# Kernel tuning notes

Measured on AMD Instinct MI355X. Metric: run time of the kernel, lower is better.

Reference implementation:

```python
import jax, jax.numpy as jnp
import numpy as np

N = 2_097_152
EPS = 1e-6


def _tri(x):
    # triangleWave (period 2), maps R -> [0, 1]; applied to 'normalize=True' tables
    return 2.0 * jnp.abs(x / 2.0 - jnp.floor(x / 2.0 + 0.5))


def _grid2d(uv, table, bilinear, normalize):
    # uv: (N,2) in [0,1); table: (U,V,L)
    t = _tri(table) if normalize else table
    U, V, _ = t.shape
    u = jnp.clip(uv[:, 0], 0.0, 1.0 - EPS) * (U - 1)
    v = jnp.clip(uv[:, 1], 0.0, 1.0 - EPS) * (V - 1)
    if bilinear:
        u0 = jnp.floor(u)
        v0 = jnp.floor(v)
        fu = (u - u0)[:, None]
        fv = (v - v0)[:, None]
        u0i = u0.astype(jnp.int32)
        v0i = v0.astype(jnp.int32)
        u1i = jnp.minimum(u0i + 1, U - 1)
        v1i = jnp.minimum(v0i + 1, V - 1)
        return (t[u0i, v0i] * (1 - fu) * (1 - fv)
                + t[u1i, v0i] * fu * (1 - fv)
                + t[u0i, v1i] * (1 - fu) * fv
                + t[u1i, v1i] * fu * fv)
    return t[jnp.round(u).astype(jnp.int32), jnp.round(v).astype(jnp.int32)]


def _grid1d(u, table, bilinear, normalize):
    # u: (N,) in [0,1); table: (U,L)
    t = _tri(table) if normalize else table
    U, _ = t.shape
    uu = jnp.clip(u, 0.0, 1.0 - EPS) * (U - 1)
    if bilinear:
        u0 = jnp.floor(uu)
        fu = (uu - u0)[:, None]
        u0i = u0.astype(jnp.int32)
        u1i = jnp.minimum(u0i + 1, U - 1)
        return t[u0i] * (1 - fu) + t[u1i] * fu
    return t[jnp.round(uu).astype(jnp.int32)]


def setup_inputs() -> dict:
    key = jax.random.key(0)
    ks = jax.random.split(key, 17)
    mk = lambda i, shape: jax.random.uniform(ks[i], shape, dtype=jnp.float32)
    names = ["roughNoh", "anisoToh", "nDotLV", "tDotLV", "metalLoh",
             "subCg", "spst", "shst", "lumCs"]
    d = {n: mk(i, (N, 2)) for i, n in enumerate(names)}
    d["tabRAEnc"] = mk(9, (2048, 2048, 2))
    d["tabCgEnc"] = mk(10, (2048, 1))
    d["tabRSEnc"] = mk(11, (64, 64, 3))
    d["tabRADec"] = mk(12, (48, 48, 3))
    d["tabCgDec"] = mk(13, (96, 2))
    d["tabLVR"] = mk(14, (32, 32, 1))
    d["tabLV"] = mk(15, (32, 32, 4))
    d["tabNHL"] = mk(16, (32, 32, 4))
    return d


def reference(roughNoh, anisoToh, nDotLV, tDotLV, metalLoh, subCg, spst, shst,
              lumCs, tabRAEnc, tabCgEnc, tabRSEnc, tabRADec, tabCgDec,
              tabLVR, tabLV, tabNHL):
    raIn = jnp.stack((roughNoh[:, 0], anisoToh[:, 0]), axis=1)  # (N,2)
    metallicity = metalLoh[:, 0]
    # ---- encoder: LUT lookups + elementwise mixing coefficients ----
    ra = _grid2d(raIn, tabRAEnc, bilinear=False, normalize=True)           # (N,2)
    cg = _grid1d(subCg[:, 1], tabCgEnc, bilinear=False, normalize=True)    # (N,1)
    rsEnc = _grid2d(jnp.concatenate((raIn[:, 0:1], subCg[:, 0:1]), axis=1),
                    tabRSEnc, bilinear=True, normalize=True)               # (N,3)
    cd = (1 - metallicity) * lumCs[:, 0]
    cm0 = (spst[:, 0] * 0.1 * (1 - metallicity) * spst[:, 1]
           + metallicity * lumCs[:, 0])[:, None]
    cm1 = (spst[:, 0] * 0.1 * (1 - metallicity) * (1 - spst[:, 1]))[:, None]
    cs0 = (shst[:, 0] * (1 - metallicity) * shst[:, 1])[:, None]
    cs1 = (shst[:, 0] * (1 - metallicity) * (1 - shst[:, 1]))[:, None]
    cc = (0.25 * 0.25 * lumCs[:, 1])[:, None]
    rsCd = rsEnc * cd[:, None]                                             # (N,3)
    # ---- decoder LUTs ----
    raCoefs = _grid2d(ra, tabRADec, bilinear=True, normalize=False)        # (N,3)
    cgCoefs = _grid1d(cg[:, 0], tabCgDec, bilinear=True, normalize=False)  # (N,2)
    vTerm = _grid2d(jnp.concatenate((nDotLV[:, 0:1] * nDotLV[:, 1:2],
                                     ra[:, 0:1]), axis=1),
                    tabLVR, bilinear=True, normalize=True)                 # (N,1)
    nlvCoefs = _grid2d(nDotLV, tabLV, bilinear=True, normalize=True)       # (N,4)
    nhlCoefs = _grid2d(jnp.stack((metalLoh[:, 1], nDotLV[:, 0]), axis=1),
                       tabNHL, bilinear=True, normalize=True)              # (N,4)
    # ---- elementwise shading combination ----
    noh2 = roughNoh[:, 1] ** 2
    den = raCoefs[:, 0] * anisoToh[:, 1] ** 2 + raCoefs[:, 1] * noh2 + raCoefs[:, 2]
    dTerm = (0.25 / (nDotLV[:, 1] * den ** 2))[:, None]
    x = (rsCd[:, 0:1] * metalLoh[:, 1:2] * nlvCoefs[:, 1:2]
         + rsCd[:, 1:2] * nlvCoefs[:, 2:3]
         + rsCd[:, 2:3] * nlvCoefs[:, 3:4]
         + cm0 * vTerm * nhlCoefs[:, 2:3] * dTerm
         + cs0 * nhlCoefs[:, 0:1])
    y = (((1 - cm1) * nhlCoefs[:, 3:4] + cm1) * vTerm * dTerm
         + cs1 * nhlCoefs[:, 0:1]
         + cc * nhlCoefs[:, 1:2] * nlvCoefs[:, 0:1]
           / (nDotLV[:, 1] * (cgCoefs[:, 0] * noh2 + cgCoefs[:, 1]))[:, None])
    return jnp.concatenate((x, y), axis=1)  # (N,2)
```

## Files before the change

### kernel.cpp

```cpp
#include <hip/hip_runtime.h>
#include <hip/hip_fp16.h>

#define CLIP_HI (1.0f - 1e-6f)

typedef float f4v __attribute__((ext_vector_type(4)));

__device__ __forceinline__ float tri_(float x) {
    return 2.0f * fabsf(x * 0.5f - floorf(x * 0.5f + 0.5f));
}

__device__ __forceinline__ float clamp01(float x) {
    return fminf(fmaxf(x, 0.0f), CLIP_HI);
}

__device__ __forceinline__ float4 nt_load4(const float* p) {
    f4v v = __builtin_nontemporal_load((const f4v*)p);
    return make_float4(v.x, v.y, v.z, v.w);
}
__device__ __forceinline__ void nt_store4(float* p, float4 v) {
    f4v t = {v.x, v.y, v.z, v.w};
    __builtin_nontemporal_store(t, (f4v*)p);
}

struct H4 { __half2 xy, zw; };

struct BW {
    int i00, i10, i01, i11;
    float w00, w10, w01, w11;
};

template <int U, int V>
__device__ __forceinline__ BW bw2d(float uc, float vc) {
    float u = clamp01(uc) * (float)(U - 1);
    float v = clamp01(vc) * (float)(V - 1);
    float u0f = floorf(u), v0f = floorf(v);
    float fu = u - u0f, fv = v - v0f;
    int u0 = (int)u0f, v0 = (int)v0f;
    int u1 = min(u0 + 1, U - 1);
    int v1 = min(v0 + 1, V - 1);
    BW r;
    r.i00 = u0 * V + v0;
    r.i10 = u1 * V + v0;
    r.i01 = u0 * V + v1;
    r.i11 = u1 * V + v1;
    float gu = 1.0f - fu, gv = 1.0f - fv;
    r.w00 = gu * gv; r.w10 = fu * gv; r.w01 = gu * fv; r.w11 = fu * fv;
    return r;
}

__device__ __forceinline__ float4 h4_blend(H4 A, H4 B, H4 C, H4 D, const BW& b) {
    float2 Axy = __half22float2(A.xy), Azw = __half22float2(A.zw);
    float2 Bxy = __half22float2(B.xy), Bzw = __half22float2(B.zw);
    float2 Cxy = __half22float2(C.xy), Czw = __half22float2(C.zw);
    float2 Dxy = __half22float2(D.xy), Dzw = __half22float2(D.zw);
    return make_float4(
        Axy.x * b.w00 + Bxy.x * b.w10 + Cxy.x * b.w01 + Dxy.x * b.w11,
        Axy.y * b.w00 + Bxy.y * b.w10 + Cxy.y * b.w01 + Dxy.y * b.w11,
        Azw.x * b.w00 + Bzw.x * b.w10 + Czw.x * b.w01 + Dzw.x * b.w11,
        Azw.y * b.w00 + Bzw.y * b.w10 + Czw.y * b.w01 + Dzw.y * b.w11);
}

__global__ __launch_bounds__(256) void prep_rs_kernel(const float* __restrict__ t,
                                                      H4* __restrict__ o) {
    int j = blockIdx.x * 256 + threadIdx.x;
    if (j < 64 * 64) {
        float a = tri_(t[j * 3 + 0]);
        float b = tri_(t[j * 3 + 1]);
        float c = tri_(t[j * 3 + 2]);
        H4 h;
        h.xy = __floats2half2_rn(a, b);
        h.zw = __floats2half2_rn(c, 0.0f);
        o[j] = h;
    }
}

template <bool USE_WS>
__device__ __forceinline__ float2 shade(
    float rNx, float rNy, float aTx, float aTy, float nLVx, float nLVy,
    float mLx, float mLy, float sCx, float sCy, float spx, float spy,
    float shx, float shy, float lCx, float lCy,
    const float* __restrict__ tabRAEnc, const float* __restrict__ tabRSEnc,
    const H4* __restrict__ rsPacked,
    const float* sRADec, const float2* sCgDec, const float* sCgEnc,
    const float* sLVR, const H4* sLV, const H4* sNHL)
{
    int ui = (int)rintf(clamp01(rNx) * 2047.0f);
    int vi = (int)rintf(clamp01(aTx) * 2047.0f);
    float2 raT = ((const float2*)tabRAEnc)[ui * 2048 + vi];

    float rs0, rs1, rs2;
    {
        BW b = bw2d<64, 64>(rNx, sCx);
        if constexpr (USE_WS) {
            float4 r = h4_blend(rsPacked[b.i00], rsPacked[b.i10],
                                rsPacked[b.i01], rsPacked[b.i11], b);
            rs0 = r.x; rs1 = r.y; rs2 = r.z;
        } else {
            const float* p00 = tabRSEnc + b.i00 * 3;
            const float* p10 = tabRSEnc + b.i10 * 3;
            const float* p01 = tabRSEnc + b.i01 * 3;
            const float* p11 = tabRSEnc + b.i11 * 3;
            rs0 = tri_(p00[0]) * b.w00 + tri_(p10[0]) * b.w10 + tri_(p01[0]) * b.w01 + tri_(p11[0]) * b.w11;
            rs1 = tri_(p00[1]) * b.w00 + tri_(p10[1]) * b.w10 + tri_(p01[1]) * b.w01 + tri_(p11[1]) * b.w11;
            rs2 = tri_(p00[2]) * b.w00 + tri_(p10[2]) * b.w10 + tri_(p01[2]) * b.w01 + tri_(p11[2]) * b.w11;
        }
    }

    float cgC0, cgC1;
    {
        float cg = sCgEnc[(int)rintf(clamp01(sCy) * 2047.0f)];
        float u = clamp01(cg) * 95.0f;
        float u0f = floorf(u);
        float fu = u - u0f;
        int u0 = (int)u0f;
        int u1 = min(u0 + 1, 95);
        float2 a = sCgDec[u0];
        float2 b = sCgDec[u1];
        cgC0 = a.x * (1.0f - fu) + b.x * fu;
        cgC1 = a.y * (1.0f - fu) + b.y * fu;
    }

    float4 nlv, nhl;
    {
        BW b = bw2d<32, 32>(nLVx, nLVy);
        nlv = h4_blend(sLV[b.i00], sLV[b.i10], sLV[b.i01], sLV[b.i11], b);
    }
    {
        BW b = bw2d<32, 32>(mLy, nLVx);
        nhl = h4_blend(sNHL[b.i00], sNHL[b.i10], sNHL[b.i01], sNHL[b.i11], b);
    }

    float ra0 = tri_(raT.x);
    float ra1 = tri_(raT.y);

    float raC0, raC1, raC2;
    {
        BW b = bw2d<48, 48>(ra0, ra1);
        const float* p00 = &sRADec[b.i00 * 3];
        const float* p10 = &sRADec[b.i10 * 3];
        const float* p01 = &sRADec[b.i01 * 3];
        const float* p11 = &sRADec[b.i11 * 3];
        raC0 = p00[0] * b.w00 + p10[0] * b.w10 + p01[0] * b.w01 + p11[0] * b.w11;
        raC1 = p00[1] * b.w00 + p10[1] * b.w10 + p01[1] * b.w01 + p11[1] * b.w11;
        raC2 = p00[2] * b.w00 + p10[2] * b.w10 + p01[2] * b.w01 + p11[2] * b.w11;
    }

    float vTerm;
    {
        BW b = bw2d<32, 32>(nLVx * nLVy, ra0);
        vTerm = sLVR[b.i00] * b.w00 + sLVR[b.i10] * b.w10 +
                sLVR[b.i01] * b.w01 + sLVR[b.i11] * b.w11;
    }

    float met = mLx;
    float om  = 1.0f - met;
    float cd  = om * lCx;
    float cm0 = spx * 0.1f * om * spy + met * lCx;
    float cm1 = spx * 0.1f * om * (1.0f - spy);
    float cs0 = shx * om * shy;
    float cs1 = shx * om * (1.0f - shy);
    float cc  = 0.0625f * lCy;

    float noh2 = rNy * rNy;
    float den  = raC0 * aTy * aTy + raC1 * noh2 + raC2;
    float dTerm = 0.25f / (nLVy * den * den);

    float x = rs0 * cd * mLy * nlv.y + rs1 * cd * nlv.z + rs2 * cd * nlv.w
            + cm0 * vTerm * nhl.z * dTerm + cs0 * nhl.x;

    float y = ((1.0f - cm1) * nhl.w + cm1) * vTerm * dTerm
            + cs1 * nhl.x
            + cc * nhl.y * nlv.x / (nLVy * (cgC0 * noh2 + cgC1));

    return make_float2(x, y);
}

template <bool USE_WS>
__global__ __launch_bounds__(1024, 8) void disney_main(
    const float* __restrict__ roughNoh,
    const float* __restrict__ anisoToh,
    const float* __restrict__ nDotLV,
    const float* __restrict__ metalLoh,
    const float* __restrict__ subCg,
    const float* __restrict__ spst,
    const float* __restrict__ shst,
    const float* __restrict__ lumCs,
    const float* __restrict__ tabRAEnc,
    const float* __restrict__ tabCgEnc,
    const float* __restrict__ tabRSEnc,
    const H4*    __restrict__ rsPacked,
    const float* __restrict__ tabRADec,
    const float* __restrict__ tabCgDec,
    const float* __restrict__ tabLVR,
    const float* __restrict__ tabLV,
    const float* __restrict__ tabNHL,
    float* __restrict__ out,
    int n)
{
    __shared__ float  sRADec[48 * 48 * 3];
    __shared__ float2 sCgDec[96];
    __shared__ float  sCgEnc[2048];
    __shared__ float  sLVR[1024];
    __shared__ H4     sLV[1024];
    __shared__ H4     sNHL[1024];

    int tid = threadIdx.x;

    for (int j = tid; j < 48 * 48 * 3; j += 1024) sRADec[j] = tabRADec[j];
    if (tid < 96) sCgDec[tid] = ((const float2*)tabCgDec)[tid];
    sCgEnc[tid]        = tri_(tabCgEnc[tid]);
    sCgEnc[tid + 1024] = tri_(tabCgEnc[tid + 1024]);
    sLVR[tid] = tri_(tabLVR[tid]);
    {
        float4 v = ((const float4*)tabLV)[tid];
        H4 h; h.xy = __floats2half2_rn(tri_(v.x), tri_(v.y));
              h.zw = __floats2half2_rn(tri_(v.z), tri_(v.w));
        sLV[tid] = h;
    }
    {
        float4 v = ((const float4*)tabNHL)[tid];
        H4 h; h.xy = __floats2half2_rn(tri_(v.x), tri_(v.y));
              h.zw = __floats2half2_rn(tri_(v.z), tri_(v.w));
        sNHL[tid] = h;
    }
    __syncthreads();

    int p = blockIdx.x * 1024 + tid;
    int e0 = 2 * p;
    if (e0 >= n) return;
    bool has2 = (e0 + 1) < n;

    float4 rN  = nt_load4(roughNoh + 4 * p);
    float4 aT  = nt_load4(anisoToh + 4 * p);
    float4 nLV = nt_load4(nDotLV   + 4 * p);
    float4 mL  = nt_load4(metalLoh + 4 * p);
    float4 sC  = nt_load4(subCg    + 4 * p);
    float4 sp  = nt_load4(spst     + 4 * p);
    float4 sh  = nt_load4(shst     + 4 * p);
    float4 lC  = nt_load4(lumCs    + 4 * p);

    float2 r0 = shade<USE_WS>(rN.x, rN.y, aT.x, aT.y, nLV.x, nLV.y,
                              mL.x, mL.y, sC.x, sC.y, sp.x, sp.y,
                              sh.x, sh.y, lC.x, lC.y,
                              tabRAEnc, tabRSEnc, rsPacked,
                              sRADec, sCgDec, sCgEnc, sLVR, sLV, sNHL);
    if (has2) {
        float2 r1 = shade<USE_WS>(rN.z, rN.w, aT.z, aT.w, nLV.z, nLV.w,
                                  mL.z, mL.w, sC.z, sC.w, sp.z, sp.w,
                                  sh.z, sh.w, lC.z, lC.w,
                                  tabRAEnc, tabRSEnc, rsPacked,
                                  sRADec, sCgDec, sCgEnc, sLVR, sLV, sNHL);
        nt_store4(out + 4 * p, make_float4(r0.x, r0.y, r1.x, r1.y));
    } else {
        ((float2*)out)[e0] = r0;
    }
}

extern "C" void kernel_launch(void* const* d_in, const int* in_sizes, int n_in,
                              void* d_out, int out_size, void* d_ws, size_t ws_size,
                              hipStream_t stream) {
    const float* roughNoh = (const float*)d_in[0];
    const float* anisoToh = (const float*)d_in[1];
    const float* nDotLV   = (const float*)d_in[2];
    const float* metalLoh = (const float*)d_in[4];
    const float* subCg    = (const float*)d_in[5];
    const float* spst     = (const float*)d_in[6];
    const float* shst     = (const float*)d_in[7];
    const float* lumCs    = (const float*)d_in[8];
    const float* tabRAEnc = (const float*)d_in[9];
    const float* tabCgEnc = (const float*)d_in[10];
    const float* tabRSEnc = (const float*)d_in[11];
    const float* tabRADec = (const float*)d_in[12];
    const float* tabCgDec = (const float*)d_in[13];
    const float* tabLVR   = (const float*)d_in[14];
    const float* tabLV    = (const float*)d_in[15];
    const float* tabNHL   = (const float*)d_in[16];

    int n = in_sizes[0] / 2;
    float* out = (float*)d_out;

    const int block = 1024;
    int pairs = (n + 1) / 2;
    int grid = (pairs + block - 1) / block;

    bool use_ws = ws_size >= (size_t)(64 * 64 * sizeof(H4));
    if (use_ws) {
        prep_rs_kernel<<<(64 * 64 + 255) / 256, 256, 0, stream>>>(tabRSEnc, (H4*)d_ws);
        disney_main<true><<<grid, block, 0, stream>>>(
            roughNoh, anisoToh, nDotLV, metalLoh, subCg, spst, shst, lumCs,
            tabRAEnc, tabCgEnc, tabRSEnc, (const H4*)d_ws,
            tabRADec, tabCgDec, tabLVR, tabLV, tabNHL, out, n);
    } else {
        disney_main<false><<<grid, block, 0, stream>>>(
            roughNoh, anisoToh, nDotLV, metalLoh, subCg, spst, shst, lumCs,
            tabRAEnc, tabCgEnc, tabRSEnc, (const H4*)d_ws,
            tabRADec, tabCgDec, tabLVR, tabLV, tabNHL, out, n);
    }
}
```

Measured before the change: 267.6 us.

## Process four elements per thread, hoist RA gathers, precompose Cg tables

Each thread now handles four elements and issues all four large-table RA gathers up front, so their memory latency overlaps with each other and with the remaining streaming loads. The two-stage Cg lookup (encode then 1D decode) is collapsed into a single precomputed 2048-entry float2 shared table built per block. The grid is halved, which reduces the per-block shared-table setup cost relative to useful work, at the price of more registers per thread and fewer resident threads to hide latency.

```diff
diff --git a/kernel.cpp b/kernel.cpp
--- a/kernel.cpp
+++ b/kernel.cpp
@@ -74,20 +74,23 @@
     }
 }
 
+__device__ __forceinline__ float2 gatherRA(const float* __restrict__ tabRAEnc,
+                                           float rNx, float aTx) {
+    int ui = (int)rintf(clamp01(rNx) * 2047.0f);
+    int vi = (int)rintf(clamp01(aTx) * 2047.0f);
+    return ((const float2*)tabRAEnc)[ui * 2048 + vi];
+}
+
 template <bool USE_WS>
-__device__ __forceinline__ float2 shade(
-    float rNx, float rNy, float aTx, float aTy, float nLVx, float nLVy,
+__device__ __forceinline__ float2 shadeB(
+    float rNx, float rNy, float aTy, float nLVx, float nLVy,
     float mLx, float mLy, float sCx, float sCy, float spx, float spy,
     float shx, float shy, float lCx, float lCy,
-    const float* __restrict__ tabRAEnc, const float* __restrict__ tabRSEnc,
-    const H4* __restrict__ rsPacked,
-    const float* sRADec, const float2* sCgDec, const float* sCgEnc,
-    const float* sLVR, const H4* sLV, const H4* sNHL)
+    float2 raT,
+    const float* __restrict__ tabRSEnc, const H4* __restrict__ rsPacked,
+    const float* sRADec, const float2* sCgComp, const float* sLVR,
+    const H4* sLV, const H4* sNHL)
 {
-    int ui = (int)rintf(clamp01(rNx) * 2047.0f);
-    int vi = (int)rintf(clamp01(aTx) * 2047.0f);
-    float2 raT = ((const float2*)tabRAEnc)[ui * 2048 + vi];
-
     float rs0, rs1, rs2;
     {
         BW b = bw2d<64, 64>(rNx, sCx);
@@ -106,19 +109,7 @@
         }
     }
 
-    float cgC0, cgC1;
-    {
-        float cg = sCgEnc[(int)rintf(clamp01(sCy) * 2047.0f)];
-        float u = clamp01(cg) * 95.0f;
-        float u0f = floorf(u);
-        float fu = u - u0f;
-        int u0 = (int)u0f;
-        int u1 = min(u0 + 1, 95);
-        float2 a = sCgDec[u0];
-        float2 b = sCgDec[u1];
-        cgC0 = a.x * (1.0f - fu) + b.x * fu;
-        cgC1 = a.y * (1.0f - fu) + b.y * fu;
-    }
+    float2 cgC = sCgComp[(int)rintf(clamp01(sCy) * 2047.0f)];
 
     float4 nlv, nhl;
     {
@@ -170,7 +161,7 @@
 
     float y = ((1.0f - cm1) * nhl.w + cm1) * vTerm * dTerm
             + cs1 * nhl.x
-            + cc * nhl.y * nlv.x / (nLVy * (cgC0 * noh2 + cgC1));
+            + cc * nhl.y * nlv.x / (nLVy * (cgC.x * noh2 + cgC.y));
 
     return make_float2(x, y);
 }
@@ -198,8 +189,7 @@
     int n)
 {
     __shared__ float  sRADec[48 * 48 * 3];
-    __shared__ float2 sCgDec[96];
-    __shared__ float  sCgEnc[2048];
+    __shared__ float2 sCgComp[2048];
     __shared__ float  sLVR[1024];
     __shared__ H4     sLV[1024];
     __shared__ H4     sNHL[1024];
@@ -207,9 +197,20 @@
     int tid = threadIdx.x;
 
     for (int j = tid; j < 48 * 48 * 3; j += 1024) sRADec[j] = tabRADec[j];
-    if (tid < 96) sCgDec[tid] = ((const float2*)tabCgDec)[tid];
-    sCgEnc[tid]        = tri_(tabCgEnc[tid]);
-    sCgEnc[tid + 1024] = tri_(tabCgEnc[tid + 1024]);
+#pragma unroll
+    for (int k = 0; k < 2; ++k) {
+        int j = tid + k * 1024;
+        float cg = tri_(tabCgEnc[j]);
+        float u = clamp01(cg) * 95.0f;
+        float u0f = floorf(u);
+        float fu = u - u0f;
+        int u0 = (int)u0f;
+        int u1 = min(u0 + 1, 95);
+        float2 a = ((const float2*)tabCgDec)[u0];
+        float2 b = ((const float2*)tabCgDec)[u1];
+        sCgComp[j] = make_float2(a.x * (1.0f - fu) + b.x * fu,
+                                 a.y * (1.0f - fu) + b.y * fu);
+    }
     sLVR[tid] = tri_(tabLVR[tid]);
     {
         float4 v = ((const float4*)tabLV)[tid];
@@ -225,34 +226,77 @@
     }
     __syncthreads();
 
-    int p = blockIdx.x * 1024 + tid;
-    int e0 = 2 * p;
+    int g = blockIdx.x * 1024 + tid;
+    int e0 = 4 * g;
     if (e0 >= n) return;
-    bool has2 = (e0 + 1) < n;
-
-    float4 rN  = nt_load4(roughNoh + 4 * p);
-    float4 aT  = nt_load4(anisoToh + 4 * p);
-    float4 nLV = nt_load4(nDotLV   + 4 * p);
-    float4 mL  = nt_load4(metalLoh + 4 * p);
-    float4 sC  = nt_load4(subCg    + 4 * p);
-    float4 sp  = nt_load4(spst     + 4 * p);
-    float4 sh  = nt_load4(shst     + 4 * p);
-    float4 lC  = nt_load4(lumCs    + 4 * p);
-
-    float2 r0 = shade<USE_WS>(rN.x, rN.y, aT.x, aT.y, nLV.x, nLV.y,
-                              mL.x, mL.y, sC.x, sC.y, sp.x, sp.y,
-                              sh.x, sh.y, lC.x, lC.y,
-                              tabRAEnc, tabRSEnc, rsPacked,
-                              sRADec, sCgDec, sCgEnc, sLVR, sLV, sNHL);
-    if (has2) {
-        float2 r1 = shade<USE_WS>(rN.z, rN.w, aT.z, aT.w, nLV.z, nLV.w,
-                                  mL.z, mL.w, sC.z, sC.w, sp.z, sp.w,
-                                  sh.z, sh.w, lC.z, lC.w,
-                                  tabRAEnc, tabRSEnc, rsPacked,
-                                  sRADec, sCgDec, sCgEnc, sLVR, sLV, sNHL);
-        nt_store4(out + 4 * p, make_float4(r0.x, r0.y, r1.x, r1.y));
+
+    if (e0 + 3 < n) {
+        float4 rNa = nt_load4(roughNoh + 8 * g);
+        float4 rNb = nt_load4(roughNoh + 8 * g + 4);
+        float4 aTa = nt_load4(anisoToh + 8 * g);
+        float4 aTb = nt_load4(anisoToh + 8 * g + 4);
+
+        float2 raT0 = gatherRA(tabRAEnc, rNa.x, aTa.x);
+        float2 raT1 = gatherRA(tabRAEnc, rNa.z, aTa.z);
+        float2 raT2 = gatherRA(tabRAEnc, rNb.x, aTb.x);
+        float2 raT3 = gatherRA(tabRAEnc, rNb.z, aTb.z);
+
+        {
+            float4 nLV = nt_load4(nDotLV   + 8 * g);
+            float4 mL  = nt_load4(metalLoh + 8 * g);
+            float4 sC  = nt_load4(subCg    + 8 * g);
+            float4 sp  = nt_load4(spst     + 8 * g);
+            float4 sh  = nt_load4(shst     + 8 * g);
+            float4 lC  = nt_load4(lumCs    + 8 * g);
+            float2 r0 = shadeB<USE_WS>(rNa.x, rNa.y, aTa.y, nLV.x, nLV.y,
+                                       mL.x, mL.y, sC.x, sC.y, sp.x, sp.y,
+                                       sh.x, sh.y, lC.x, lC.y, raT0,
+                                       tabRSEnc, rsPacked,
+                                       sRADec, sCgComp, sLVR, sLV, sNHL);
+            float2 r1 = shadeB<USE_WS>(rNa.z, rNa.w, aTa.w, nLV.z, nLV.w,
+                                       mL.z, mL.w, sC.z, sC.w, sp.z, sp.w,
+                                       sh.z, sh.w, lC.z, lC.w, raT1,
+                                       tabRSEnc, rsPacked,
+                                       sRADec, sCgComp, sLVR, sLV, sNHL);
+            nt_store4(out + 8 * g, make_float4(r0.x, r0.y, r1.x, r1.y));
+        }
+        {
+            float4 nLV = nt_load4(nDotLV   + 8 * g + 4);
+            float4 mL  = nt_load4(metalLoh + 8 * g + 4);
+            float4 sC  = nt_load4(subCg    + 8 * g + 4);
+            float4 sp  = nt_load4(spst     + 8 * g + 4);
+            float4 sh  = nt_load4(shst     + 8 * g + 4);
+            float4 lC  = nt_load4(lumCs    + 8 * g + 4);
+            float2 r2 = shadeB<USE_WS>(rNb.x, rNb.y, aTb.y, nLV.x, nLV.y,
+                                       mL.x, mL.y, sC.x, sC.y, sp.x, sp.y,
+                                       sh.x, sh.y, lC.x, lC.y, raT2,
+                                       tabRSEnc, rsPacked,
+                                       sRADec, sCgComp, sLVR, sLV, sNHL);
+            float2 r3 = shadeB<USE_WS>(rNb.z, rNb.w, aTb.w, nLV.z, nLV.w,
+                                       mL.z, mL.w, sC.z, sC.w, sp.z, sp.w,
+                                       sh.z, sh.w, lC.z, lC.w, raT3,
+                                       tabRSEnc, rsPacked,
+                                       sRADec, sCgComp, sLVR, sLV, sNHL);
+            nt_store4(out + 8 * g + 4, make_float4(r2.x, r2.y, r3.x, r3.y));
+        }
     } else {
-        ((float2*)out)[e0] = r0;
+        for (int e = e0; e < n; ++e) {
+            float2 rN  = ((const float2*)roughNoh)[e];
+            float2 aT  = ((const float2*)anisoToh)[e];
+            float2 nLV = ((const float2*)nDotLV)[e];
+            float2 mL  = ((const float2*)metalLoh)[e];
+            float2 sC  = ((const float2*)subCg)[e];
+            float2 sp  = ((const float2*)spst)[e];
+            float2 sh  = ((const float2*)shst)[e];
+            float2 lC  = ((const float2*)lumCs)[e];
+            float2 raT = gatherRA(tabRAEnc, rN.x, aT.x);
+            float2 r = shadeB<USE_WS>(rN.x, rN.y, aT.y, nLV.x, nLV.y,
+                                      mL.x, mL.y, sC.x, sC.y, sp.x, sp.y,
+                                      sh.x, sh.y, lC.x, lC.y, raT,
+                                      tabRSEnc, rsPacked,
+                                      sRADec, sCgComp, sLVR, sLV, sNHL);
+            ((float2*)out)[e] = r;
+        }
     }
 }
 
@@ -280,8 +324,8 @@
     float* out = (float*)d_out;
 
     const int block = 1024;
-    int pairs = (n + 1) / 2;
-    int grid = (pairs + block - 1) / block;
+    int groups = (n + 3) / 4;
+    int grid = (groups + block - 1) / block;
 
     bool use_ws = ws_size >= (size_t)(64 * 64 * sizeof(H4));
     if (use_ws) {
```

New measurement: 298.6 us. 11.6% more time.
